# Kernel optimization log

Measured on AMD Instinct MI355X. Metric: run time of the kernel, lower is better.

## Reference

```python
import jax, jax.numpy as jnp
import numpy as np

L, N, Q, F, P, H, C = 2, 4, 8, 8, 257, 12, 64
K = F * P  # 2056
WIDTH = H * C  # 768


def layernorm(x, g, b, eps=1e-5):
    x32 = x.astype(jnp.float32)
    mu = x32.mean(-1, keepdims=True)
    var = x32.var(-1, keepdims=True)
    return ((x32 - mu) * jax.lax.rsqrt(var + eps) * g + b).astype(x.dtype)


def smax(q, k, m, num_frames):
    # q:[n,q,h,c] k:[n,k,h,c] m:[n,k] bool
    c = q.shape[-1]
    aff = jnp.einsum('nqhc,nkhc->nqkh', q / jnp.sqrt(jnp.float32(c)), k)
    aff = jnp.where(m[:, None, :, None], aff, -jnp.inf)
    n, ql, kl, h = aff.shape
    a_patch = jax.nn.softmax(aff, axis=-2)
    aff_f = aff.reshape(n, ql, num_frames, kl // num_frames, h)
    a_frame = jax.nn.softmax(aff_f, axis=-2).reshape(n, ql, kl, h)
    a_temp = jax.nn.softmax(aff_f, axis=-3).reshape(n, ql, kl, h)
    return (a_patch + a_frame + a_temp) / 3.0


def coda(q, k, m):
    c = q.shape[-1]
    norm = jnp.sqrt(jnp.float32(c))
    aff = jnp.tanh(jnp.einsum('nqhc,nkhc->nqkh', q / norm, k))
    # pairwise L1 distance gate: [n,q,k,h]
    gate = -jnp.abs(q[:, :, None] - k[:, None]).sum(-1) / norm
    gate = 2.0 * jax.nn.sigmoid(gate)
    gate = jnp.where(m[:, None, :, None], gate, 0.0)
    return aff * gate


def quick_gelu(x):
    return x * jax.nn.sigmoid(1.702 * x)


def setup_inputs() -> dict:
    key = jax.random.key(0)
    ks = jax.random.split(key, 8)
    s = 0.02
    return {
        'x': jax.random.normal(ks[0], (N, Q, WIDTH), jnp.float32),
        'k': jax.random.normal(ks[1], (L, N, K, H, C), jnp.float32),
        'v': jax.random.normal(ks[2], (L, N, K, H, C), jnp.float32),
        'm': jnp.ones((N, K), dtype=bool),
        'in_proj_w': s * jax.random.normal(ks[3], (L, 2 * WIDTH, WIDTH), jnp.float32),
        'out_proj_w': s * jax.random.normal(ks[4], (L, WIDTH, WIDTH), jnp.float32),
        'ln1_g': jnp.ones((L, WIDTH), jnp.float32),
        'ln1_b': jnp.zeros((L, WIDTH), jnp.float32),
        'ln2_g': jnp.ones((L, WIDTH), jnp.float32),
        'ln2_b': jnp.zeros((L, WIDTH), jnp.float32),
        'fc_w': s * jax.random.normal(ks[5], (L, 4 * WIDTH, WIDTH), jnp.float32),
        'fc_b': jnp.zeros((L, 4 * WIDTH), jnp.float32),
        'proj_w': s * jax.random.normal(ks[6], (L, WIDTH, 4 * WIDTH), jnp.float32),
        'proj_b': jnp.zeros((L, WIDTH), jnp.float32),
        'num_frames': F,
    }


def reference(x, k, v, m, in_proj_w, out_proj_w, ln1_g, ln1_b, ln2_g, ln2_b,
              fc_w, fc_b, proj_w, proj_b, num_frames):
    n, ql, width = x.shape
    n_layers = k.shape[0]
    h = k.shape[3]
    c = width // h
    results = []
    for i in range(n_layers):
        qn = layernorm(x, ln1_g[i], ln1_b[i])
        qp = (qn @ in_proj_w[i].T).reshape(n, ql, h, 2 * c)
        q0, q1 = qp[..., :c], qp[..., c:]
        aff = (smax(q0, k[i], m, num_frames) + coda(q1, k[i], m)) / 2.0
        mix = jnp.einsum('nqkh,nkhc->nqhc', aff, v[i]).reshape(n, ql, width)
        x = x + mix @ out_proj_w[i].T
        xn = layernorm(x, ln2_g[i], ln2_b[i])
        hdn = quick_gelu(xn @ fc_w[i].T + fc_b[i])
        x = x + hdn @ proj_w[i].T + proj_b[i]
        results.append(x)
    return jnp.stack(results, axis=1)  # [n, L, q, width]
```

## Files before the change

kernel.cpp:

```cpp
#include <hip/hip_runtime.h>
#include <math.h>

namespace {
constexpr int LL = 2, NN = 4, QQ = 8, FF = 8, PP = 257, HH = 12, CC = 64;
constexpr int KK = FF * PP;
constexpr int WD = HH * CC;
constexpr int MM = NN * QQ;
constexpr int NHQK = NN * HH * QQ * KK;
constexpr int NHQ  = NN * HH * QQ;
constexpr int NHQF = NHQ * FF;
constexpr int NHQP = NHQ * PP;
constexpr int KC_MIX = 33;
constexpr int ATS = 776;

typedef float f32x4 __attribute__((ext_vector_type(4)));
typedef short bf16x8 __attribute__((ext_vector_type(8)));

__device__ inline short bfr(float f) {
    unsigned u = __float_as_uint(f);
    return (short)((u + 0x7fffu + ((u >> 16) & 1u)) >> 16);
}
__device__ inline short4 bfr4(float4 v) {
    short4 s; s.x = bfr(v.x); s.y = bfr(v.y); s.z = bfr(v.z); s.w = bfr(v.w); return s;
}
__device__ inline float safe_tanh(float x) {
    float e = __expf(2.f * fabsf(x));
    float th = 1.f - 2.f / (e + 1.f);
    return x < 0.f ? -th : th;
}
__device__ inline float qgelu(float v) { return v / (1.f + __expf(-1.702f * v)); }

template <int KCH>
__device__ inline void gemm_core(const short (*At)[ATS], const float* __restrict__ W,
                                 int K, int Ncols, float* __restrict__ part_out, int bx)
{
    int t = threadIdx.x, l = t & 63, w = t >> 6;
    int r = l & 15, s = l >> 4;
    int n0 = bx * 64 + w * 16;
    f32x4 acc0 = {0.f, 0.f, 0.f, 0.f}, acc1 = {0.f, 0.f, 0.f, 0.f};
    const float* wb = W + (size_t)(n0 + r) * K + s * 8;
#pragma unroll
    for (int kc = 0; kc < KCH / 32; ++kc) {
        const float* p = wb + kc * 32;
        float4 u = *(const float4*)p, v = *(const float4*)(p + 4);
        bf16x8 bf;
        bf[0]=bfr(u.x); bf[1]=bfr(u.y); bf[2]=bfr(u.z); bf[3]=bfr(u.w);
        bf[4]=bfr(v.x); bf[5]=bfr(v.y); bf[6]=bfr(v.z); bf[7]=bfr(v.w);
        bf16x8 a0 = *(const bf16x8*)&At[r][kc * 32 + s * 8];
        bf16x8 a1 = *(const bf16x8*)&At[r + 16][kc * 32 + s * 8];
        acc0 = __builtin_amdgcn_mfma_f32_16x16x32_bf16(a0, bf, acc0, 0, 0, 0);
        acc1 = __builtin_amdgcn_mfma_f32_16x16x32_bf16(a1, bf, acc1, 0, 0, 0);
    }
    float* ob = part_out + n0 + r;
#pragma unroll
    for (int i = 0; i < 4; ++i) {
        ob[(size_t)(s * 4 + i) * Ncols]      = acc0[i];
        ob[(size_t)(16 + s * 4 + i) * Ncols] = acc1[i];
    }
}

template <int MODE, int NSUM, int KCH>
__global__ void lngemm(const float* __restrict__ xsrc,
                       const float* __restrict__ addpart,
                       const float* __restrict__ colbias,
                       float* __restrict__ xstore,
                       float* __restrict__ outstore, int layer,
                       const float* __restrict__ g, const float* __restrict__ bb,
                       const float* __restrict__ W,
                       float* __restrict__ part, int Ncols)
{
    __shared__ short At[32][ATS];
    __shared__ float rsum[32][8], rss[32][8];
    __shared__ float lmu[32], linv[32];
    int t = threadIdx.x, r = t >> 3, l = t & 7;
    int k0 = blockIdx.y * KCH;
    bool writer = (MODE != 0) && blockIdx.x == 0 && blockIdx.y == 0;
    float s = 0.f, ss = 0.f;
    for (int j = 0; j < 24; ++j) {
        int c = (l + j * 8) * 4;
        float4 xv = *(const float4*)(xsrc + (size_t)r * WD + c);
        if (NSUM > 0) {
#pragma unroll
            for (int p = 0; p < NSUM; ++p) {
                float4 a = *(const float4*)(addpart + ((size_t)p * MM + r) * WD + c);
                xv.x += a.x; xv.y += a.y; xv.z += a.z; xv.w += a.w;
            }
        }
        if (MODE == 2) {
            float4 cb = *(const float4*)(colbias + c);
            xv.x += cb.x; xv.y += cb.y; xv.z += cb.z; xv.w += cb.w;
        }
        if (writer) {
            *(float4*)(xstore + (size_t)r * WD + c) = xv;
            if (MODE == 2) {
                int n = r >> 3, q = r & 7;
                *(float4*)(outstore + (((size_t)n * LL + layer) * QQ + q) * WD + c) = xv;
            }
        }
        s  += xv.x + xv.y + xv.z + xv.w;
        ss += xv.x * xv.x + xv.y * xv.y + xv.z * xv.z + xv.w * xv.w;
    }
    rsum[r][l] = s; rss[r][l] = ss;
    __syncthreads();
    if (t < 32) {
        float a = 0.f, b2 = 0.f;
#pragma unroll
        for (int i = 0; i < 8; ++i) { a += rsum[t][i]; b2 += rss[t][i]; }
        float mu = a * (1.f / WD);
        float var = b2 * (1.f / WD) - mu * mu;
        lmu[t] = mu; linv[t] = rsqrtf(var + 1e-5f);
    }
    __syncthreads();
    float mu = lmu[r], inv = linv[r];
    for (int j = 0; j < KCH / 32; ++j) {
        int c = k0 + (l + j * 8) * 4;
        float4 xv = *(const float4*)(xsrc + (size_t)r * WD + c);
        if (NSUM > 0) {
#pragma unroll
            for (int p = 0; p < NSUM; ++p) {
                float4 a = *(const float4*)(addpart + ((size_t)p * MM + r) * WD + c);
                xv.x += a.x; xv.y += a.y; xv.z += a.z; xv.w += a.w;
            }
        }
        if (MODE == 2) {
            float4 cb = *(const float4*)(colbias + c);
            xv.x += cb.x; xv.y += cb.y; xv.z += cb.z; xv.w += cb.w;
        }
        float4 gg = *(const float4*)(g + c), bv = *(const float4*)(bb + c);
        float4 nv;
        nv.x = (xv.x - mu) * inv * gg.x + bv.x;
        nv.y = (xv.y - mu) * inv * gg.y + bv.y;
        nv.z = (xv.z - mu) * inv * gg.z + bv.z;
        nv.w = (xv.w - mu) * inv * gg.w + bv.w;
        *(short4*)&At[r][c - k0] = bfr4(nv);
    }
    __syncthreads();
    gemm_core<KCH>(At, W + k0, WD, Ncols,
                   part + (size_t)blockIdx.y * MM * Ncols, blockIdx.x);
}

__global__ void sumgemm(const float* __restrict__ parts,
                        const float* __restrict__ W,
                        float* __restrict__ part)
{
    __shared__ short At[32][ATS];
    int t = threadIdx.x, r = t >> 3, l = t & 7;
    int k0 = blockIdx.y * 192;
    for (int j = 0; j < 6; ++j) {
        int c = k0 + (l + j * 8) * 4;
        float4 sv = make_float4(0.f, 0.f, 0.f, 0.f);
        for (int ch = 0; ch < KC_MIX; ++ch) {
            float4 a = *(const float4*)(parts + ((size_t)ch * MM + r) * WD + c);
            sv.x += a.x; sv.y += a.y; sv.z += a.z; sv.w += a.w;
        }
        *(short4*)&At[r][c - k0] = bfr4(sv);
    }
    __syncthreads();
    gemm_core<192>(At, W + k0, WD, WD,
                   part + (size_t)blockIdx.y * MM * WD, blockIdx.x);
}

__global__ void actgemm(const float* __restrict__ parts,
                        const float* __restrict__ fbias,
                        const float* __restrict__ W,
                        float* __restrict__ part)
{
    __shared__ short At[32][ATS];
    int t = threadIdx.x, r = t >> 3, l = t & 7;
    int k0 = blockIdx.y * 384;
    for (int j = 0; j < 12; ++j) {
        int c = k0 + (l + j * 8) * 4;
        float4 a = *(const float4*)(parts + (size_t)r * 3072 + c);
        float4 b = *(const float4*)(parts + ((size_t)MM + r) * 3072 + c);
        float4 fb = *(const float4*)(fbias + c);
        float4 v;
        v.x = qgelu(a.x + b.x + fb.x);
        v.y = qgelu(a.y + b.y + fb.y);
        v.z = qgelu(a.z + b.z + fb.z);
        v.w = qgelu(a.w + b.w + fb.w);
        *(short4*)&At[r][c - k0] = bfr4(v);
    }
    __syncthreads();
    gemm_core<384>(At, W + k0, 3072, WD,
                   part + (size_t)blockIdx.y * MM * WD, blockIdx.x);
}

template <int NPART>
__global__ void scores_kernel(const float* __restrict__ kmat,
                              const float* __restrict__ qparts,
                              float* __restrict__ S0,
                              float* __restrict__ SC)
{
    int h = blockIdx.y, n = blockIdx.z;
    __shared__ float q0s[QQ][CC], q1s[QQ][CC];
    for (int i = threadIdx.x; i < QQ * 128; i += 256) {
        int q = i >> 7, c = i & 127;
        size_t off = ((size_t)(n * QQ + q)) * 1536 + h * 128 + c;
        float s = 0.f;
#pragma unroll
        for (int p = 0; p < NPART; ++p) s += qparts[(size_t)p * MM * 1536 + off];
        if (c < 64) q0s[q][c] = s; else q1s[q][c - 64] = s;
    }
    __syncthreads();
    int kk = blockIdx.x * 256 + threadIdx.x;
    if (kk >= KK) return;
    const float* kr = kmat + (((size_t)n * KK + kk) * HH + h) * CC;
    float4 kv[16];
#pragma unroll
    for (int j = 0; j < 16; ++j) kv[j] = *(const float4*)(kr + j * 4);
#pragma unroll 1
    for (int q = 0; q < QQ; ++q) {
        float s0 = 0.f, s1 = 0.f, g = 0.f;
#pragma unroll
        for (int j = 0; j < 16; ++j) {
            float4 a = *(const float4*)&q0s[q][j * 4];
            float4 c = *(const float4*)&q1s[q][j * 4];
            s0 += a.x * kv[j].x + a.y * kv[j].y + a.z * kv[j].z + a.w * kv[j].w;
            s1 += c.x * kv[j].x + c.y * kv[j].y + c.z * kv[j].z + c.w * kv[j].w;
            g  += fabsf(c.x - kv[j].x) + fabsf(c.y - kv[j].y) +
                  fabsf(c.z - kv[j].z) + fabsf(c.w - kv[j].w);
        }
        float gate = 2.f / (1.f + __expf(g * 0.125f));
        float sc = safe_tanh(s1 * 0.125f) * gate;
        size_t b = ((size_t)n * HH + h) * QQ + q;
        S0[b * KK + kk] = s0 * 0.125f;
        SC[b * KK + kk] = sc;
    }
}

__global__ void stats_kernel(const float* __restrict__ S0,
                             float* __restrict__ pM, float* __restrict__ pS,
                             float* __restrict__ fMv, float* __restrict__ fSv,
                             float* __restrict__ tMv, float* __restrict__ tSv)
{
    int b = blockIdx.x, t = threadIdx.x;
    const float* rowp = S0 + (size_t)b * KK;
    __shared__ float sr[KK];
    __shared__ float red[256];
    for (int i = t; i < KK; i += 256) sr[i] = rowp[i];
    __syncthreads();
    float lm = -1e30f;
    for (int i = t; i < KK; i += 256) lm = fmaxf(lm, sr[i]);
    red[t] = lm; __syncthreads();
    for (int s = 128; s; s >>= 1) { if (t < s) red[t] = fmaxf(red[t], red[t + s]); __syncthreads(); }
    float pmax = red[0]; __syncthreads();
    float ls = 0.f;
    for (int i = t; i < KK; i += 256) ls += __expf(sr[i] - pmax);
    red[t] = ls; __syncthreads();
    for (int s = 128; s; s >>= 1) { if (t < s) red[t] += red[t + s]; __syncthreads(); }
    if (t == 0) { pM[b] = pmax; pS[b] = 1.f / red[0]; }
    int f = t >> 5, l32 = t & 31;
    float fm = -1e30f;
    for (int p = l32; p < PP; p += 32) fm = fmaxf(fm, sr[f * PP + p]);
#pragma unroll
    for (int msk = 1; msk < 32; msk <<= 1) fm = fmaxf(fm, __shfl_xor(fm, msk, 64));
    float fsum = 0.f;
    for (int p = l32; p < PP; p += 32) fsum += __expf(sr[f * PP + p] - fm);
#pragma unroll
    for (int msk = 1; msk < 32; msk <<= 1) fsum += __shfl_xor(fsum, msk, 64);
    if (l32 == 0) { fMv[b * FF + f] = fm; fSv[b * FF + f] = 1.f / fsum; }
    for (int p = t; p < PP; p += 256) {
        float tm = -1e30f;
#pragma unroll
        for (int f2 = 0; f2 < FF; ++f2) tm = fmaxf(tm, sr[f2 * PP + p]);
        float tsum = 0.f;
#pragma unroll
        for (int f2 = 0; f2 < FF; ++f2) tsum += __expf(sr[f2 * PP + p] - tm);
        tMv[b * PP + p] = tm; tSv[b * PP + p] = 1.f / tsum;
    }
}

__global__ void mix_kernel(const float* __restrict__ vmat,
                           const float* __restrict__ S0, const float* __restrict__ SC,
                           const float* __restrict__ pM, const float* __restrict__ pS,
                           const float* __restrict__ fMv, const float* __restrict__ fSv,
                           const float* __restrict__ tMv, const float* __restrict__ tSv,
                           float* __restrict__ mix_part)
{
    int kc = blockIdx.x, h = blockIdx.y, n = blockIdx.z;
    int t = threadIdx.x;
    __shared__ float wtab[64][QQ];
    __shared__ float red[16][QQ][CC];
    int kk0 = kc * 64;
    for (int i = t; i < 64 * QQ; i += 256) {
        int kkl = i >> 3, q = i & 7;
        int kk = kk0 + kkl;
        float wv = 0.f;
        if (kk < KK) {
            int b = (n * HH + h) * QQ + q;
            float s0 = S0[(size_t)b * KK + kk];
            float sc = SC[(size_t)b * KK + kk];
            int f = kk / PP, p = kk - f * PP;
            float e = __expf(s0 - pM[b]) * pS[b]
                    + __expf(s0 - fMv[b * FF + f]) * fSv[b * FF + f]
                    + __expf(s0 - tMv[b * PP + p]) * tSv[b * PP + p];
            wv = 0.5f * (e * (1.f / 3.f) + sc);
        }
        wtab[kkl][q] = wv;
    }
    __syncthreads();
    int c4 = t & 15, kg = t >> 4;
    float4 acc[QQ];
#pragma unroll
    for (int q = 0; q < QQ; ++q) acc[q] = make_float4(0.f, 0.f, 0.f, 0.f);
#pragma unroll
    for (int it = 0; it < 4; ++it) {
        int kkl = it * 16 + kg;
        int kk = kk0 + kkl;
        if (kk < KK) {
            float4 vv = *(const float4*)&vmat[(((size_t)n * KK + kk) * HH + h) * CC + c4 * 4];
#pragma unroll
            for (int q = 0; q < QQ; ++q) {
                float wv = wtab[kkl][q];
                acc[q].x += wv * vv.x; acc[q].y += wv * vv.y;
                acc[q].z += wv * vv.z; acc[q].w += wv * vv.w;
            }
        }
    }
#pragma unroll
    for (int q = 0; q < QQ; ++q) *(float4*)&red[kg][q][c4 * 4] = acc[q];
    __syncthreads();
    for (int i = t; i < QQ * CC / 4; i += 256) {
        int q = i >> 4, c4i = i & 15;
        float4 s = make_float4(0.f, 0.f, 0.f, 0.f);
#pragma unroll
        for (int g = 0; g < 16; ++g) {
            float4 p = *(float4*)&red[g][q][c4i * 4];
            s.x += p.x; s.y += p.y; s.z += p.z; s.w += p.w;
        }
        *(float4*)&mix_part[((size_t)kc * MM + n * QQ + q) * WD + h * CC + c4i * 4] = s;
    }
}

__global__ void final_kernel(const float* __restrict__ x2,
                             const float* __restrict__ pparts,
                             const float* __restrict__ pb,
                             float* __restrict__ outp, int layer)
{
    int m = blockIdx.x, t = threadIdx.x;
    int n = m >> 3, q = m & 7;
    for (int c = t; c < WD; c += 256) {
        float v = x2[(size_t)m * WD + c] + pb[c];
#pragma unroll
        for (int p2 = 0; p2 < 8; ++p2) v += pparts[((size_t)p2 * MM + m) * WD + c];
        outp[(((size_t)n * LL + layer) * QQ + q) * WD + c] = v;
    }
}
}

extern "C" void kernel_launch(void* const* d_in, const int* in_sizes, int n_in,
                              void* d_out, int out_size, void* d_ws, size_t ws_size,
                              hipStream_t stream) {
    const float* x_in  = (const float*)d_in[0];
    const float* k_in  = (const float*)d_in[1];
    const float* v_in  = (const float*)d_in[2];
    const float* inw   = (const float*)d_in[4];
    const float* outw  = (const float*)d_in[5];
    const float* ln1g  = (const float*)d_in[6];
    const float* ln1b  = (const float*)d_in[7];
    const float* ln2g  = (const float*)d_in[8];
    const float* ln2b  = (const float*)d_in[9];
    const float* fcw   = (const float*)d_in[10];
    const float* fcb   = (const float*)d_in[11];
    const float* pjw   = (const float*)d_in[12];
    const float* pjb   = (const float*)d_in[13];
    float* out = (float*)d_out;
    float* ws  = (float*)d_ws;

    float* qp_part  = ws;
    float* S0       = qp_part + 4 * MM * 1536;
    float* SC       = S0 + NHQK;
    float* pM       = SC + NHQK;
    float* pS       = pM + NHQ;
    float* fMv      = pS + NHQ;
    float* fSv      = fMv + NHQF;
    float* tMv      = fSv + NHQF;
    float* tSv      = tMv + NHQP;
    float* mix_part = tSv + NHQP;
    float* op_part  = mix_part + KC_MIX * MM * WD;
    float* fc_part  = op_part + 4 * MM * WD;
    float* pj_part  = fc_part + 2 * MM * 3072;
    float* x2buf    = pj_part + 8 * MM * WD;
    float* x3buf    = x2buf + MM * WD;

    for (int i = 0; i < LL; ++i) {
        const float* kl = k_in + (size_t)i * NN * KK * HH * CC;
        const float* vl = v_in + (size_t)i * NN * KK * HH * CC;

        if (i == 0) {
            lngemm<0, 0, 192><<<dim3(24, 4), 256, 0, stream>>>(
                x_in, nullptr, nullptr, nullptr, nullptr, 0,
                ln1g, ln1b, inw, qp_part, 1536);
        } else {
            lngemm<2, 8, 192><<<dim3(24, 4), 256, 0, stream>>>(
                x2buf, pj_part, pjb, x3buf, out, 0,
                ln1g + WD, ln1b + WD, inw + (size_t)1536 * WD, qp_part, 1536);
        }
        scores_kernel<4><<<dim3(9, HH, NN), 256, 0, stream>>>(kl, qp_part, S0, SC);
        stats_kernel<<<NHQ, 256, 0, stream>>>(S0, pM, pS, fMv, fSv, tMv, tSv);
        mix_kernel<<<dim3(KC_MIX, HH, NN), 256, 0, stream>>>(
            vl, S0, SC, pM, pS, fMv, fSv, tMv, tSv, mix_part);
        sumgemm<<<dim3(12, 4), 256, 0, stream>>>(
            mix_part, outw + (size_t)i * WD * WD, op_part);
        lngemm<1, 4, 384><<<dim3(48, 2), 256, 0, stream>>>(
            (i == 0) ? x_in : x3buf, op_part, nullptr, x2buf, nullptr, 0,
            ln2g + i * WD, ln2b + i * WD, fcw + (size_t)i * 3072 * WD, fc_part, 3072);
        actgemm<<<dim3(12, 8), 256, 0, stream>>>(
            fc_part, fcb + (size_t)i * 3072, pjw + (size_t)i * WD * 3072, pj_part);
        if (i == LL - 1) {
            final_kernel<<<MM, 256, 0, stream>>>(x2buf, pj_part, pjb + WD, out, 1);
        }
    }
}
```

Before: 388.3 us.

## Fuse all layer stages into one persistent kernel with grid barriers

Replaces the sequence of per-stage kernel launches with a single persistent kernel of 256 blocks that walks through every stage of both layers, separating stages with an atomic-counter grid barrier. GEMM stages are re-split into 192 blocks with smaller K chunks, so more partial sums are produced and reduced in later stages, and residual updates move into separate small stages. This aims to remove launch gaps and give the small GEMMs more parallelism. In exchange it adds a barrier after every stage, more partial-sum traffic, and relies on all 256 blocks being co-resident.

```diff
diff --git a/kernel.cpp b/kernel.cpp
--- a/kernel.cpp
+++ b/kernel.cpp
@@ -10,8 +10,7 @@
 constexpr int NHQ  = NN * HH * QQ;
 constexpr int NHQF = NHQ * FF;
 constexpr int NHQP = NHQ * PP;
-constexpr int KC_MIX = 33;
-constexpr int ATS = 776;
+constexpr int GRIDB = 256;
 
 typedef float f32x4 __attribute__((ext_vector_type(4)));
 typedef short bf16x8 __attribute__((ext_vector_type(8)));
@@ -30,320 +29,350 @@
 }
 __device__ inline float qgelu(float v) { return v / (1.f + __expf(-1.702f * v)); }
 
+struct SMg  { short At[32][200]; float rsum[32][8]; float rss[32][8]; float mu[32]; float inv[32]; };
+struct SMsc { float q0[QQ][CC]; float q1[QQ][CC]; };
+struct SMst { float sr[KK]; float red[256]; };
+struct SMmx { float wtab[64][QQ]; float red[16][QQ][CC]; };
+union  SMu  { SMg g; SMsc sc; SMst st; SMmx mx; };
+
+struct MP {
+    const float *xin, *kin, *vin;
+    const float *inw, *outw, *ln1g, *ln1b, *ln2g, *ln2b, *fcw, *fcb, *pjw, *pjb;
+    float *out;
+    unsigned *bar;
+    float *qp_part, *S0, *SC, *pM, *pS, *fMv, *fSv, *tMv, *tSv;
+    float *mix_part, *op_part, *fc_part, *pj_part, *x2, *x3;
+};
+
+__device__ inline void gsync(unsigned* bar, unsigned& epoch)
+{
+    __syncthreads();
+    if (threadIdx.x == 0) {
+        epoch += GRIDB;
+        __threadfence();
+        __hip_atomic_fetch_add(bar, 1u, __ATOMIC_ACQ_REL, __HIP_MEMORY_SCOPE_AGENT);
+        while (__hip_atomic_load(bar, __ATOMIC_ACQUIRE, __HIP_MEMORY_SCOPE_AGENT) < epoch)
+            __builtin_amdgcn_s_sleep(2);
+        __threadfence();
+    }
+    __syncthreads();
+}
+
 template <int KCH>
-__device__ inline void gemm_core(const short (*At)[ATS], const float* __restrict__ W,
-                                 int K, int Ncols, float* __restrict__ part_out, int bx)
+__device__ inline void gemm_core(const SMu& sm, const float* __restrict__ W,
+                                 int K, int Ncols, float* __restrict__ po, int bx, int t)
 {
-    int t = threadIdx.x, l = t & 63, w = t >> 6;
-    int r = l & 15, s = l >> 4;
+    int l = t & 63, w = t >> 6, r = l & 15, s = l >> 4;
     int n0 = bx * 64 + w * 16;
-    f32x4 acc0 = {0.f, 0.f, 0.f, 0.f}, acc1 = {0.f, 0.f, 0.f, 0.f};
+    f32x4 a0 = {0.f, 0.f, 0.f, 0.f}, a1 = {0.f, 0.f, 0.f, 0.f};
     const float* wb = W + (size_t)(n0 + r) * K + s * 8;
 #pragma unroll
     for (int kc = 0; kc < KCH / 32; ++kc) {
-        const float* p = wb + kc * 32;
-        float4 u = *(const float4*)p, v = *(const float4*)(p + 4);
-        bf16x8 bf;
-        bf[0]=bfr(u.x); bf[1]=bfr(u.y); bf[2]=bfr(u.z); bf[3]=bfr(u.w);
-        bf[4]=bfr(v.x); bf[5]=bfr(v.y); bf[6]=bfr(v.z); bf[7]=bfr(v.w);
-        bf16x8 a0 = *(const bf16x8*)&At[r][kc * 32 + s * 8];
-        bf16x8 a1 = *(const bf16x8*)&At[r + 16][kc * 32 + s * 8];
-        acc0 = __builtin_amdgcn_mfma_f32_16x16x32_bf16(a0, bf, acc0, 0, 0, 0);
-        acc1 = __builtin_amdgcn_mfma_f32_16x16x32_bf16(a1, bf, acc1, 0, 0, 0);
-    }
-    float* ob = part_out + n0 + r;
+        const float* pp = wb + kc * 32;
+        float4 u = *(const float4*)pp, v = *(const float4*)(pp + 4);
+        bf16x8 bw;
+        bw[0]=bfr(u.x); bw[1]=bfr(u.y); bw[2]=bfr(u.z); bw[3]=bfr(u.w);
+        bw[4]=bfr(v.x); bw[5]=bfr(v.y); bw[6]=bfr(v.z); bw[7]=bfr(v.w);
+        bf16x8 fa0 = *(const bf16x8*)&sm.g.At[r][kc * 32 + s * 8];
+        bf16x8 fa1 = *(const bf16x8*)&sm.g.At[r + 16][kc * 32 + s * 8];
+        a0 = __builtin_amdgcn_mfma_f32_16x16x32_bf16(fa0, bw, a0, 0, 0, 0);
+        a1 = __builtin_amdgcn_mfma_f32_16x16x32_bf16(fa1, bw, a1, 0, 0, 0);
+    }
+    float* ob = po + n0 + r;
 #pragma unroll
     for (int i = 0; i < 4; ++i) {
-        ob[(size_t)(s * 4 + i) * Ncols]      = acc0[i];
-        ob[(size_t)(16 + s * 4 + i) * Ncols] = acc1[i];
-    }
-}
-
-template <int MODE, int NSUM, int KCH>
-__global__ void lngemm(const float* __restrict__ xsrc,
-                       const float* __restrict__ addpart,
-                       const float* __restrict__ colbias,
-                       float* __restrict__ xstore,
-                       float* __restrict__ outstore, int layer,
-                       const float* __restrict__ g, const float* __restrict__ bb,
-                       const float* __restrict__ W,
-                       float* __restrict__ part, int Ncols)
+        ob[(size_t)(s * 4 + i) * Ncols]      = a0[i];
+        ob[(size_t)(16 + s * 4 + i) * Ncols] = a1[i];
+    }
+}
+
+__device__ inline void ln_stats(SMu& sm, const float* __restrict__ x, int t)
 {
-    __shared__ short At[32][ATS];
-    __shared__ float rsum[32][8], rss[32][8];
-    __shared__ float lmu[32], linv[32];
-    int t = threadIdx.x, r = t >> 3, l = t & 7;
-    int k0 = blockIdx.y * KCH;
-    bool writer = (MODE != 0) && blockIdx.x == 0 && blockIdx.y == 0;
+    int r = t >> 3, l = t & 7;
     float s = 0.f, ss = 0.f;
     for (int j = 0; j < 24; ++j) {
         int c = (l + j * 8) * 4;
-        float4 xv = *(const float4*)(xsrc + (size_t)r * WD + c);
-        if (NSUM > 0) {
-#pragma unroll
-            for (int p = 0; p < NSUM; ++p) {
-                float4 a = *(const float4*)(addpart + ((size_t)p * MM + r) * WD + c);
-                xv.x += a.x; xv.y += a.y; xv.z += a.z; xv.w += a.w;
-            }
-        }
-        if (MODE == 2) {
-            float4 cb = *(const float4*)(colbias + c);
-            xv.x += cb.x; xv.y += cb.y; xv.z += cb.z; xv.w += cb.w;
-        }
-        if (writer) {
-            *(float4*)(xstore + (size_t)r * WD + c) = xv;
-            if (MODE == 2) {
-                int n = r >> 3, q = r & 7;
-                *(float4*)(outstore + (((size_t)n * LL + layer) * QQ + q) * WD + c) = xv;
-            }
-        }
+        float4 xv = *(const float4*)(x + (size_t)r * WD + c);
         s  += xv.x + xv.y + xv.z + xv.w;
         ss += xv.x * xv.x + xv.y * xv.y + xv.z * xv.z + xv.w * xv.w;
     }
-    rsum[r][l] = s; rss[r][l] = ss;
+    sm.g.rsum[r][l] = s; sm.g.rss[r][l] = ss;
     __syncthreads();
     if (t < 32) {
         float a = 0.f, b2 = 0.f;
 #pragma unroll
-        for (int i = 0; i < 8; ++i) { a += rsum[t][i]; b2 += rss[t][i]; }
+        for (int i = 0; i < 8; ++i) { a += sm.g.rsum[t][i]; b2 += sm.g.rss[t][i]; }
         float mu = a * (1.f / WD);
-        float var = b2 * (1.f / WD) - mu * mu;
-        lmu[t] = mu; linv[t] = rsqrtf(var + 1e-5f);
+        sm.g.mu[t] = mu;
+        sm.g.inv[t] = rsqrtf(b2 * (1.f / WD) - mu * mu + 1e-5f);
     }
     __syncthreads();
-    float mu = lmu[r], inv = linv[r];
-    for (int j = 0; j < KCH / 32; ++j) {
-        int c = k0 + (l + j * 8) * 4;
-        float4 xv = *(const float4*)(xsrc + (size_t)r * WD + c);
-        if (NSUM > 0) {
-#pragma unroll
-            for (int p = 0; p < NSUM; ++p) {
-                float4 a = *(const float4*)(addpart + ((size_t)p * MM + r) * WD + c);
-                xv.x += a.x; xv.y += a.y; xv.z += a.z; xv.w += a.w;
-            }
-        }
-        if (MODE == 2) {
-            float4 cb = *(const float4*)(colbias + c);
-            xv.x += cb.x; xv.y += cb.y; xv.z += cb.z; xv.w += cb.w;
-        }
-        float4 gg = *(const float4*)(g + c), bv = *(const float4*)(bb + c);
-        float4 nv;
-        nv.x = (xv.x - mu) * inv * gg.x + bv.x;
-        nv.y = (xv.y - mu) * inv * gg.y + bv.y;
-        nv.z = (xv.z - mu) * inv * gg.z + bv.z;
-        nv.w = (xv.w - mu) * inv * gg.w + bv.w;
-        *(short4*)&At[r][c - k0] = bfr4(nv);
-    }
-    __syncthreads();
-    gemm_core<KCH>(At, W + k0, WD, Ncols,
-                   part + (size_t)blockIdx.y * MM * Ncols, blockIdx.x);
-}
-
-__global__ void sumgemm(const float* __restrict__ parts,
-                        const float* __restrict__ W,
-                        float* __restrict__ part)
+}
+
+__global__ void __launch_bounds__(256, 1) detector_mega(MP p)
 {
-    __shared__ short At[32][ATS];
-    int t = threadIdx.x, r = t >> 3, l = t & 7;
-    int k0 = blockIdx.y * 192;
-    for (int j = 0; j < 6; ++j) {
-        int c = k0 + (l + j * 8) * 4;
-        float4 sv = make_float4(0.f, 0.f, 0.f, 0.f);
-        for (int ch = 0; ch < KC_MIX; ++ch) {
-            float4 a = *(const float4*)(parts + ((size_t)ch * MM + r) * WD + c);
-            sv.x += a.x; sv.y += a.y; sv.z += a.z; sv.w += a.w;
-        }
-        *(short4*)&At[r][c - k0] = bfr4(sv);
-    }
-    __syncthreads();
-    gemm_core<192>(At, W + k0, WD, WD,
-                   part + (size_t)blockIdx.y * MM * WD, blockIdx.x);
-}
-
-__global__ void actgemm(const float* __restrict__ parts,
-                        const float* __restrict__ fbias,
-                        const float* __restrict__ W,
-                        float* __restrict__ part)
-{
-    __shared__ short At[32][ATS];
-    int t = threadIdx.x, r = t >> 3, l = t & 7;
-    int k0 = blockIdx.y * 384;
-    for (int j = 0; j < 12; ++j) {
-        int c = k0 + (l + j * 8) * 4;
-        float4 a = *(const float4*)(parts + (size_t)r * 3072 + c);
-        float4 b = *(const float4*)(parts + ((size_t)MM + r) * 3072 + c);
-        float4 fb = *(const float4*)(fbias + c);
-        float4 v;
-        v.x = qgelu(a.x + b.x + fb.x);
-        v.y = qgelu(a.y + b.y + fb.y);
-        v.z = qgelu(a.z + b.z + fb.z);
-        v.w = qgelu(a.w + b.w + fb.w);
-        *(short4*)&At[r][c - k0] = bfr4(v);
-    }
-    __syncthreads();
-    gemm_core<384>(At, W + k0, 3072, WD,
-                   part + (size_t)blockIdx.y * MM * WD, blockIdx.x);
-}
-
-template <int NPART>
-__global__ void scores_kernel(const float* __restrict__ kmat,
-                              const float* __restrict__ qparts,
-                              float* __restrict__ S0,
-                              float* __restrict__ SC)
-{
-    int h = blockIdx.y, n = blockIdx.z;
-    __shared__ float q0s[QQ][CC], q1s[QQ][CC];
-    for (int i = threadIdx.x; i < QQ * 128; i += 256) {
-        int q = i >> 7, c = i & 127;
-        size_t off = ((size_t)(n * QQ + q)) * 1536 + h * 128 + c;
-        float s = 0.f;
-#pragma unroll
-        for (int p = 0; p < NPART; ++p) s += qparts[(size_t)p * MM * 1536 + off];
-        if (c < 64) q0s[q][c] = s; else q1s[q][c - 64] = s;
-    }
-    __syncthreads();
-    int kk = blockIdx.x * 256 + threadIdx.x;
-    if (kk >= KK) return;
-    const float* kr = kmat + (((size_t)n * KK + kk) * HH + h) * CC;
-    float4 kv[16];
-#pragma unroll
-    for (int j = 0; j < 16; ++j) kv[j] = *(const float4*)(kr + j * 4);
+    __shared__ SMu sm;
+    const int blk = blockIdx.x, t = threadIdx.x;
+    unsigned epoch = 0;
+
+    for (int layer = 0; layer < LL; ++layer) {
+        const float* xbuf = layer ? p.x3 : p.xin;
+        const size_t koff = (size_t)layer * NN * KK * HH * CC;
+        const float* kl = p.kin + koff;
+        const float* vl = p.vin + koff;
+
+        if (blk < 192) {
+            int bx = blk % 24, ky = blk / 24, k0 = ky * 96;
+            ln_stats(sm, xbuf, t);
+            {
+                int r = t >> 3, l = t & 7;
+                float mu = sm.g.mu[r], inv = sm.g.inv[r];
+                const float* g_ = p.ln1g + (size_t)layer * WD;
+                const float* b_ = p.ln1b + (size_t)layer * WD;
+#pragma unroll
+                for (int j = 0; j < 3; ++j) {
+                    int c = k0 + (l + j * 8) * 4;
+                    float4 xv = *(const float4*)(xbuf + (size_t)r * WD + c);
+                    float4 gg = *(const float4*)(g_ + c), bv = *(const float4*)(b_ + c);
+                    float4 nv;
+                    nv.x = (xv.x - mu) * inv * gg.x + bv.x;
+                    nv.y = (xv.y - mu) * inv * gg.y + bv.y;
+                    nv.z = (xv.z - mu) * inv * gg.z + bv.z;
+                    nv.w = (xv.w - mu) * inv * gg.w + bv.w;
+                    *(short4*)&sm.g.At[r][c - k0] = bfr4(nv);
+                }
+            }
+            __syncthreads();
+            gemm_core<96>(sm, p.inw + (size_t)layer * 1536 * WD + k0, WD, 1536,
+                          p.qp_part + (size_t)ky * MM * 1536, bx, t);
+        }
+        gsync(p.bar, epoch);
+
+        for (int u = blk; u < 9 * HH * NN; u += GRIDB) {
+            int kc = u % 9, rem = u / 9, h = rem % HH, n = rem / HH;
+            __syncthreads();
+            for (int i = t; i < QQ * 128; i += 256) {
+                int q = i >> 7, c = i & 127;
+                size_t off = (size_t)(n * QQ + q) * 1536 + h * 128 + c;
+                float s = 0.f;
+#pragma unroll
+                for (int pt = 0; pt < 8; ++pt) s += p.qp_part[(size_t)pt * MM * 1536 + off];
+                if (c < 64) sm.sc.q0[q][c] = s; else sm.sc.q1[q][c - 64] = s;
+            }
+            __syncthreads();
+            int kk = kc * 256 + t;
+            if (kk < KK) {
+                const float* kr = kl + (((size_t)n * KK + kk) * HH + h) * CC;
+                float4 kv[16];
+#pragma unroll
+                for (int j = 0; j < 16; ++j) kv[j] = *(const float4*)(kr + j * 4);
 #pragma unroll 1
-    for (int q = 0; q < QQ; ++q) {
-        float s0 = 0.f, s1 = 0.f, g = 0.f;
-#pragma unroll
-        for (int j = 0; j < 16; ++j) {
-            float4 a = *(const float4*)&q0s[q][j * 4];
-            float4 c = *(const float4*)&q1s[q][j * 4];
-            s0 += a.x * kv[j].x + a.y * kv[j].y + a.z * kv[j].z + a.w * kv[j].w;
-            s1 += c.x * kv[j].x + c.y * kv[j].y + c.z * kv[j].z + c.w * kv[j].w;
-            g  += fabsf(c.x - kv[j].x) + fabsf(c.y - kv[j].y) +
-                  fabsf(c.z - kv[j].z) + fabsf(c.w - kv[j].w);
-        }
-        float gate = 2.f / (1.f + __expf(g * 0.125f));
-        float sc = safe_tanh(s1 * 0.125f) * gate;
-        size_t b = ((size_t)n * HH + h) * QQ + q;
-        S0[b * KK + kk] = s0 * 0.125f;
-        SC[b * KK + kk] = sc;
-    }
-}
-
-__global__ void stats_kernel(const float* __restrict__ S0,
-                             float* __restrict__ pM, float* __restrict__ pS,
-                             float* __restrict__ fMv, float* __restrict__ fSv,
-                             float* __restrict__ tMv, float* __restrict__ tSv)
-{
-    int b = blockIdx.x, t = threadIdx.x;
-    const float* rowp = S0 + (size_t)b * KK;
-    __shared__ float sr[KK];
-    __shared__ float red[256];
-    for (int i = t; i < KK; i += 256) sr[i] = rowp[i];
-    __syncthreads();
-    float lm = -1e30f;
-    for (int i = t; i < KK; i += 256) lm = fmaxf(lm, sr[i]);
-    red[t] = lm; __syncthreads();
-    for (int s = 128; s; s >>= 1) { if (t < s) red[t] = fmaxf(red[t], red[t + s]); __syncthreads(); }
-    float pmax = red[0]; __syncthreads();
-    float ls = 0.f;
-    for (int i = t; i < KK; i += 256) ls += __expf(sr[i] - pmax);
-    red[t] = ls; __syncthreads();
-    for (int s = 128; s; s >>= 1) { if (t < s) red[t] += red[t + s]; __syncthreads(); }
-    if (t == 0) { pM[b] = pmax; pS[b] = 1.f / red[0]; }
-    int f = t >> 5, l32 = t & 31;
-    float fm = -1e30f;
-    for (int p = l32; p < PP; p += 32) fm = fmaxf(fm, sr[f * PP + p]);
-#pragma unroll
-    for (int msk = 1; msk < 32; msk <<= 1) fm = fmaxf(fm, __shfl_xor(fm, msk, 64));
-    float fsum = 0.f;
-    for (int p = l32; p < PP; p += 32) fsum += __expf(sr[f * PP + p] - fm);
-#pragma unroll
-    for (int msk = 1; msk < 32; msk <<= 1) fsum += __shfl_xor(fsum, msk, 64);
-    if (l32 == 0) { fMv[b * FF + f] = fm; fSv[b * FF + f] = 1.f / fsum; }
-    for (int p = t; p < PP; p += 256) {
-        float tm = -1e30f;
-#pragma unroll
-        for (int f2 = 0; f2 < FF; ++f2) tm = fmaxf(tm, sr[f2 * PP + p]);
-        float tsum = 0.f;
-#pragma unroll
-        for (int f2 = 0; f2 < FF; ++f2) tsum += __expf(sr[f2 * PP + p] - tm);
-        tMv[b * PP + p] = tm; tSv[b * PP + p] = 1.f / tsum;
-    }
-}
-
-__global__ void mix_kernel(const float* __restrict__ vmat,
-                           const float* __restrict__ S0, const float* __restrict__ SC,
-                           const float* __restrict__ pM, const float* __restrict__ pS,
-                           const float* __restrict__ fMv, const float* __restrict__ fSv,
-                           const float* __restrict__ tMv, const float* __restrict__ tSv,
-                           float* __restrict__ mix_part)
-{
-    int kc = blockIdx.x, h = blockIdx.y, n = blockIdx.z;
-    int t = threadIdx.x;
-    __shared__ float wtab[64][QQ];
-    __shared__ float red[16][QQ][CC];
-    int kk0 = kc * 64;
-    for (int i = t; i < 64 * QQ; i += 256) {
-        int kkl = i >> 3, q = i & 7;
-        int kk = kk0 + kkl;
-        float wv = 0.f;
-        if (kk < KK) {
-            int b = (n * HH + h) * QQ + q;
-            float s0 = S0[(size_t)b * KK + kk];
-            float sc = SC[(size_t)b * KK + kk];
-            int f = kk / PP, p = kk - f * PP;
-            float e = __expf(s0 - pM[b]) * pS[b]
-                    + __expf(s0 - fMv[b * FF + f]) * fSv[b * FF + f]
-                    + __expf(s0 - tMv[b * PP + p]) * tSv[b * PP + p];
-            wv = 0.5f * (e * (1.f / 3.f) + sc);
-        }
-        wtab[kkl][q] = wv;
-    }
-    __syncthreads();
-    int c4 = t & 15, kg = t >> 4;
-    float4 acc[QQ];
-#pragma unroll
-    for (int q = 0; q < QQ; ++q) acc[q] = make_float4(0.f, 0.f, 0.f, 0.f);
-#pragma unroll
-    for (int it = 0; it < 4; ++it) {
-        int kkl = it * 16 + kg;
-        int kk = kk0 + kkl;
-        if (kk < KK) {
-            float4 vv = *(const float4*)&vmat[(((size_t)n * KK + kk) * HH + h) * CC + c4 * 4];
-#pragma unroll
-            for (int q = 0; q < QQ; ++q) {
-                float wv = wtab[kkl][q];
-                acc[q].x += wv * vv.x; acc[q].y += wv * vv.y;
-                acc[q].z += wv * vv.z; acc[q].w += wv * vv.w;
-            }
-        }
-    }
-#pragma unroll
-    for (int q = 0; q < QQ; ++q) *(float4*)&red[kg][q][c4 * 4] = acc[q];
-    __syncthreads();
-    for (int i = t; i < QQ * CC / 4; i += 256) {
-        int q = i >> 4, c4i = i & 15;
-        float4 s = make_float4(0.f, 0.f, 0.f, 0.f);
-#pragma unroll
-        for (int g = 0; g < 16; ++g) {
-            float4 p = *(float4*)&red[g][q][c4i * 4];
-            s.x += p.x; s.y += p.y; s.z += p.z; s.w += p.w;
-        }
-        *(float4*)&mix_part[((size_t)kc * MM + n * QQ + q) * WD + h * CC + c4i * 4] = s;
-    }
-}
-
-__global__ void final_kernel(const float* __restrict__ x2,
-                             const float* __restrict__ pparts,
-                             const float* __restrict__ pb,
-                             float* __restrict__ outp, int layer)
-{
-    int m = blockIdx.x, t = threadIdx.x;
-    int n = m >> 3, q = m & 7;
-    for (int c = t; c < WD; c += 256) {
-        float v = x2[(size_t)m * WD + c] + pb[c];
-#pragma unroll
-        for (int p2 = 0; p2 < 8; ++p2) v += pparts[((size_t)p2 * MM + m) * WD + c];
-        outp[(((size_t)n * LL + layer) * QQ + q) * WD + c] = v;
+                for (int q = 0; q < QQ; ++q) {
+                    float s0 = 0.f, s1 = 0.f, g = 0.f;
+#pragma unroll
+                    for (int j = 0; j < 16; ++j) {
+                        float4 a = *(const float4*)&sm.sc.q0[q][j * 4];
+                        float4 c2 = *(const float4*)&sm.sc.q1[q][j * 4];
+                        s0 += a.x * kv[j].x + a.y * kv[j].y + a.z * kv[j].z + a.w * kv[j].w;
+                        s1 += c2.x * kv[j].x + c2.y * kv[j].y + c2.z * kv[j].z + c2.w * kv[j].w;
+                        g  += fabsf(c2.x - kv[j].x) + fabsf(c2.y - kv[j].y) +
+                              fabsf(c2.z - kv[j].z) + fabsf(c2.w - kv[j].w);
+                    }
+                    float gate = 2.f / (1.f + __expf(g * 0.125f));
+                    float sc = safe_tanh(s1 * 0.125f) * gate;
+                    size_t b = ((size_t)n * HH + h) * QQ + q;
+                    p.S0[b * KK + kk] = s0 * 0.125f;
+                    p.SC[b * KK + kk] = sc;
+                }
+            }
+        }
+        gsync(p.bar, epoch);
+
+        for (int u = blk; u < NHQ; u += GRIDB) {
+            __syncthreads();
+            const float* rowp = p.S0 + (size_t)u * KK;
+            for (int i = t; i < KK; i += 256) sm.st.sr[i] = rowp[i];
+            __syncthreads();
+            float lm = -1e30f;
+            for (int i = t; i < KK; i += 256) lm = fmaxf(lm, sm.st.sr[i]);
+            sm.st.red[t] = lm; __syncthreads();
+            for (int s = 128; s; s >>= 1) { if (t < s) sm.st.red[t] = fmaxf(sm.st.red[t], sm.st.red[t + s]); __syncthreads(); }
+            float pmax = sm.st.red[0]; __syncthreads();
+            float ls = 0.f;
+            for (int i = t; i < KK; i += 256) ls += __expf(sm.st.sr[i] - pmax);
+            sm.st.red[t] = ls; __syncthreads();
+            for (int s = 128; s; s >>= 1) { if (t < s) sm.st.red[t] += sm.st.red[t + s]; __syncthreads(); }
+            if (t == 0) { p.pM[u] = pmax; p.pS[u] = 1.f / sm.st.red[0]; }
+            int f = t >> 5, l32 = t & 31;
+            float fm = -1e30f;
+            for (int pp2 = l32; pp2 < PP; pp2 += 32) fm = fmaxf(fm, sm.st.sr[f * PP + pp2]);
+#pragma unroll
+            for (int msk = 1; msk < 32; msk <<= 1) fm = fmaxf(fm, __shfl_xor(fm, msk, 64));
+            float fsum = 0.f;
+            for (int pp2 = l32; pp2 < PP; pp2 += 32) fsum += __expf(sm.st.sr[f * PP + pp2] - fm);
+#pragma unroll
+            for (int msk = 1; msk < 32; msk <<= 1) fsum += __shfl_xor(fsum, msk, 64);
+            if (l32 == 0) { p.fMv[u * FF + f] = fm; p.fSv[u * FF + f] = 1.f / fsum; }
+            for (int pp2 = t; pp2 < PP; pp2 += 256) {
+                float tm = -1e30f;
+#pragma unroll
+                for (int f2 = 0; f2 < FF; ++f2) tm = fmaxf(tm, sm.st.sr[f2 * PP + pp2]);
+                float tsum = 0.f;
+#pragma unroll
+                for (int f2 = 0; f2 < FF; ++f2) tsum += __expf(sm.st.sr[f2 * PP + pp2] - tm);
+                p.tMv[u * PP + pp2] = tm; p.tSv[u * PP + pp2] = 1.f / tsum;
+            }
+        }
+        gsync(p.bar, epoch);
+
+        for (int u = blk; u < 33 * HH * NN; u += GRIDB) {
+            int kc = u % 33, rem = u / 33, h = rem % HH, n = rem / HH;
+            int kk0 = kc * 64;
+            __syncthreads();
+            for (int i = t; i < 64 * QQ; i += 256) {
+                int kkl = i >> 3, q = i & 7;
+                int kk = kk0 + kkl;
+                float wv = 0.f;
+                if (kk < KK) {
+                    int b = (n * HH + h) * QQ + q;
+                    float s0 = p.S0[(size_t)b * KK + kk];
+                    float sc = p.SC[(size_t)b * KK + kk];
+                    int f = kk / PP, pp2 = kk - f * PP;
+                    float e = __expf(s0 - p.pM[b]) * p.pS[b]
+                            + __expf(s0 - p.fMv[b * FF + f]) * p.fSv[b * FF + f]
+                            + __expf(s0 - p.tMv[b * PP + pp2]) * p.tSv[b * PP + pp2];
+                    wv = 0.5f * (e * (1.f / 3.f) + sc);
+                }
+                sm.mx.wtab[kkl][q] = wv;
+            }
+            __syncthreads();
+            int c4 = t & 15, kg = t >> 4;
+            float4 acc[QQ];
+#pragma unroll
+            for (int q = 0; q < QQ; ++q) acc[q] = make_float4(0.f, 0.f, 0.f, 0.f);
+#pragma unroll
+            for (int it = 0; it < 4; ++it) {
+                int kkl = it * 16 + kg;
+                int kk = kk0 + kkl;
+                if (kk < KK) {
+                    float4 vv = *(const float4*)&vl[(((size_t)n * KK + kk) * HH + h) * CC + c4 * 4];
+#pragma unroll
+                    for (int q = 0; q < QQ; ++q) {
+                        float wv = sm.mx.wtab[kkl][q];
+                        acc[q].x += wv * vv.x; acc[q].y += wv * vv.y;
+                        acc[q].z += wv * vv.z; acc[q].w += wv * vv.w;
+                    }
+                }
+            }
+#pragma unroll
+            for (int q = 0; q < QQ; ++q) *(float4*)&sm.mx.red[kg][q][c4 * 4] = acc[q];
+            __syncthreads();
+            for (int i = t; i < QQ * CC / 4; i += 256) {
+                int q = i >> 4, c4i = i & 15;
+                float4 s = make_float4(0.f, 0.f, 0.f, 0.f);
+#pragma unroll
+                for (int g = 0; g < 16; ++g) {
+                    float4 pr = *(float4*)&sm.mx.red[g][q][c4i * 4];
+                    s.x += pr.x; s.y += pr.y; s.z += pr.z; s.w += pr.w;
+                }
+                *(float4*)&p.mix_part[((size_t)kc * MM + n * QQ + q) * WD + h * CC + c4i * 4] = s;
+            }
+        }
+        gsync(p.bar, epoch);
+
+        if (blk < 96) {
+            int bx = blk % 12, ky = blk / 12, k0 = ky * 96;
+            int r = t >> 3, l = t & 7;
+#pragma unroll
+            for (int j = 0; j < 3; ++j) {
+                int c = k0 + (l + j * 8) * 4;
+                float4 sv = make_float4(0.f, 0.f, 0.f, 0.f);
+                for (int ch = 0; ch < 33; ++ch) {
+                    float4 a = *(const float4*)(p.mix_part + ((size_t)ch * MM + r) * WD + c);
+                    sv.x += a.x; sv.y += a.y; sv.z += a.z; sv.w += a.w;
+                }
+                *(short4*)&sm.g.At[r][c - k0] = bfr4(sv);
+            }
+            __syncthreads();
+            gemm_core<96>(sm, p.outw + (size_t)layer * WD * WD + k0, WD, WD,
+                          p.op_part + (size_t)ky * MM * WD, bx, t);
+        }
+        gsync(p.bar, epoch);
+
+        if (blk < MM) {
+            for (int c = t; c < WD; c += 256) {
+                float v = xbuf[(size_t)blk * WD + c];
+#pragma unroll
+                for (int s2 = 0; s2 < 8; ++s2) v += p.op_part[((size_t)s2 * MM + blk) * WD + c];
+                p.x2[(size_t)blk * WD + c] = v;
+            }
+        }
+        gsync(p.bar, epoch);
+
+        if (blk < 192) {
+            int bx = blk % 48, ky = blk / 48, k0 = ky * 192;
+            ln_stats(sm, p.x2, t);
+            {
+                int r = t >> 3, l = t & 7;
+                float mu = sm.g.mu[r], inv = sm.g.inv[r];
+                const float* g_ = p.ln2g + (size_t)layer * WD;
+                const float* b_ = p.ln2b + (size_t)layer * WD;
+#pragma unroll
+                for (int j = 0; j < 6; ++j) {
+                    int c = k0 + (l + j * 8) * 4;
+                    float4 xv = *(const float4*)(p.x2 + (size_t)r * WD + c);
+                    float4 gg = *(const float4*)(g_ + c), bv = *(const float4*)(b_ + c);
+                    float4 nv;
+                    nv.x = (xv.x - mu) * inv * gg.x + bv.x;
+                    nv.y = (xv.y - mu) * inv * gg.y + bv.y;
+                    nv.z = (xv.z - mu) * inv * gg.z + bv.z;
+                    nv.w = (xv.w - mu) * inv * gg.w + bv.w;
+                    *(short4*)&sm.g.At[r][c - k0] = bfr4(nv);
+                }
+            }
+            __syncthreads();
+            gemm_core<192>(sm, p.fcw + (size_t)layer * 3072 * WD + k0, WD, 3072,
+                           p.fc_part + (size_t)ky * MM * 3072, bx, t);
+        }
+        gsync(p.bar, epoch);
+
+        if (blk < 192) {
+            int bx = blk % 12, ky = blk / 12, k0 = ky * 192;
+            int r = t >> 3, l = t & 7;
+            const float* fb = p.fcb + (size_t)layer * 3072;
+#pragma unroll
+            for (int j = 0; j < 6; ++j) {
+                int c = k0 + (l + j * 8) * 4;
+                float4 a  = *(const float4*)(p.fc_part + (size_t)r * 3072 + c);
+                float4 b  = *(const float4*)(p.fc_part + ((size_t)MM + r) * 3072 + c);
+                float4 c2 = *(const float4*)(p.fc_part + ((size_t)2 * MM + r) * 3072 + c);
+                float4 d  = *(const float4*)(p.fc_part + ((size_t)3 * MM + r) * 3072 + c);
+                float4 bbv = *(const float4*)(fb + c);
+                float4 v;
+                v.x = qgelu(a.x + b.x + c2.x + d.x + bbv.x);
+                v.y = qgelu(a.y + b.y + c2.y + d.y + bbv.y);
+                v.z = qgelu(a.z + b.z + c2.z + d.z + bbv.z);
+                v.w = qgelu(a.w + b.w + c2.w + d.w + bbv.w);
+                *(short4*)&sm.g.At[r][c - k0] = bfr4(v);
+            }
+            __syncthreads();
+            gemm_core<192>(sm, p.pjw + (size_t)layer * WD * 3072 + k0, 3072, WD,
+                           p.pj_part + (size_t)ky * MM * WD, bx, t);
+        }
+        gsync(p.bar, epoch);
+
+        if (blk < MM) {
+            int n = blk >> 3, q = blk & 7;
+            const float* pb = p.pjb + (size_t)layer * WD;
+            for (int c = t; c < WD; c += 256) {
+                float v = p.x2[(size_t)blk * WD + c] + pb[c];
+#pragma unroll
+                for (int s2 = 0; s2 < 16; ++s2) v += p.pj_part[((size_t)s2 * MM + blk) * WD + c];
+                if (layer == 0) p.x3[(size_t)blk * WD + c] = v;
+                p.out[(((size_t)n * LL + layer) * QQ + q) * WD + c] = v;
+            }
+        }
+        if (layer == 0) gsync(p.bar, epoch);
     }
 }
 }
@@ -351,64 +380,40 @@
 extern "C" void kernel_launch(void* const* d_in, const int* in_sizes, int n_in,
                               void* d_out, int out_size, void* d_ws, size_t ws_size,
                               hipStream_t stream) {
-    const float* x_in  = (const float*)d_in[0];
-    const float* k_in  = (const float*)d_in[1];
-    const float* v_in  = (const float*)d_in[2];
-    const float* inw   = (const float*)d_in[4];
-    const float* outw  = (const float*)d_in[5];
-    const float* ln1g  = (const float*)d_in[6];
-    const float* ln1b  = (const float*)d_in[7];
-    const float* ln2g  = (const float*)d_in[8];
-    const float* ln2b  = (const float*)d_in[9];
-    const float* fcw   = (const float*)d_in[10];
-    const float* fcb   = (const float*)d_in[11];
-    const float* pjw   = (const float*)d_in[12];
-    const float* pjb   = (const float*)d_in[13];
-    float* out = (float*)d_out;
-    float* ws  = (float*)d_ws;
-
-    float* qp_part  = ws;
-    float* S0       = qp_part + 4 * MM * 1536;
-    float* SC       = S0 + NHQK;
-    float* pM       = SC + NHQK;
-    float* pS       = pM + NHQ;
-    float* fMv      = pS + NHQ;
-    float* fSv      = fMv + NHQF;
-    float* tMv      = fSv + NHQF;
-    float* tSv      = tMv + NHQP;
-    float* mix_part = tSv + NHQP;
-    float* op_part  = mix_part + KC_MIX * MM * WD;
-    float* fc_part  = op_part + 4 * MM * WD;
-    float* pj_part  = fc_part + 2 * MM * 3072;
-    float* x2buf    = pj_part + 8 * MM * WD;
-    float* x3buf    = x2buf + MM * WD;
-
-    for (int i = 0; i < LL; ++i) {
-        const float* kl = k_in + (size_t)i * NN * KK * HH * CC;
-        const float* vl = v_in + (size_t)i * NN * KK * HH * CC;
-
-        if (i == 0) {
-            lngemm<0, 0, 192><<<dim3(24, 4), 256, 0, stream>>>(
-                x_in, nullptr, nullptr, nullptr, nullptr, 0,
-                ln1g, ln1b, inw, qp_part, 1536);
-        } else {
-            lngemm<2, 8, 192><<<dim3(24, 4), 256, 0, stream>>>(
-                x2buf, pj_part, pjb, x3buf, out, 0,
-                ln1g + WD, ln1b + WD, inw + (size_t)1536 * WD, qp_part, 1536);
-        }
-        scores_kernel<4><<<dim3(9, HH, NN), 256, 0, stream>>>(kl, qp_part, S0, SC);
-        stats_kernel<<<NHQ, 256, 0, stream>>>(S0, pM, pS, fMv, fSv, tMv, tSv);
-        mix_kernel<<<dim3(KC_MIX, HH, NN), 256, 0, stream>>>(
-            vl, S0, SC, pM, pS, fMv, fSv, tMv, tSv, mix_part);
-        sumgemm<<<dim3(12, 4), 256, 0, stream>>>(
-            mix_part, outw + (size_t)i * WD * WD, op_part);
-        lngemm<1, 4, 384><<<dim3(48, 2), 256, 0, stream>>>(
-            (i == 0) ? x_in : x3buf, op_part, nullptr, x2buf, nullptr, 0,
-            ln2g + i * WD, ln2b + i * WD, fcw + (size_t)i * 3072 * WD, fc_part, 3072);
-        actgemm<<<dim3(12, 8), 256, 0, stream>>>(
-            fc_part, fcb + (size_t)i * 3072, pjw + (size_t)i * WD * 3072, pj_part);
-        if (i == LL - 1) {
-            final_kernel<<<MM, 256, 0, stream>>>(x2buf, pj_part, pjb + WD, out, 1);
-        }
-    }
-}
+    MP hp;
+    hp.xin  = (const float*)d_in[0];
+    hp.kin  = (const float*)d_in[1];
+    hp.vin  = (const float*)d_in[2];
+    hp.inw  = (const float*)d_in[4];
+    hp.outw = (const float*)d_in[5];
+    hp.ln1g = (const float*)d_in[6];
+    hp.ln1b = (const float*)d_in[7];
+    hp.ln2g = (const float*)d_in[8];
+    hp.ln2b = (const float*)d_in[9];
+    hp.fcw  = (const float*)d_in[10];
+    hp.fcb  = (const float*)d_in[11];
+    hp.pjw  = (const float*)d_in[12];
+    hp.pjb  = (const float*)d_in[13];
+    hp.out  = (float*)d_out;
+
+    hp.bar  = (unsigned*)d_ws;
+    float* f = (float*)d_ws + 32;
+    hp.qp_part  = f;                  f += 8  * MM * 1536;
+    hp.S0       = f;                  f += NHQK;
+    hp.SC       = f;                  f += NHQK;
+    hp.pM       = f;                  f += NHQ;
+    hp.pS       = f;                  f += NHQ;
+    hp.fMv      = f;                  f += NHQF;
+    hp.fSv      = f;                  f += NHQF;
+    hp.tMv      = f;                  f += NHQP;
+    hp.tSv      = f;                  f += NHQP;
+    hp.mix_part = f;                  f += 33 * MM * WD;
+    hp.op_part  = f;                  f += 8  * MM * WD;
+    hp.fc_part  = f;                  f += 4  * MM * 3072;
+    hp.pj_part  = f;                  f += 16 * MM * WD;
+    hp.x2       = f;                  f += MM * WD;
+    hp.x3       = f;
+
+    hipMemsetAsync(d_ws, 0, 128, stream);
+    detector_mega<<<GRIDB, 256, 0, stream>>>(hp);
+}
```

Measured after the change: 1.197 ms. +208.2%, slower.
